# Kernel tuning notes

Hardware: AMD Instinct MI355X
Metric: run time of the kernel (lower is better)

## Reference

```python
import math
import jax, jax.numpy as jnp
import numpy as np

B, T, C = 4, 2048, 1024
N_HEAD = 16
HEAD_DIM = C // N_HEAD


def setup_inputs() -> dict:
    key = jax.random.key(0)
    k1, k2, k3 = jax.random.split(key, 3)
    x = jax.random.normal(k1, (B, T, C), dtype=jnp.float32)
    # nn.Linear weights: (out_features, in_features); init scale ~1/sqrt(C)
    w_attn = jax.random.normal(k2, (3 * C, C), dtype=jnp.float32) / math.sqrt(C)
    w_proj = jax.random.normal(k3, (C, C), dtype=jnp.float32) / math.sqrt(C)
    return {"x": x, "w_attn": w_attn, "w_proj": w_proj}


def reference(x, w_attn, w_proj):
    Bx, Tx, Cx = x.shape
    qkv = x @ w_attn.T  # (B,T,3C)
    q, k, v = jnp.split(qkv, 3, axis=2)
    # (B,T,H,D) -> (B,H,T,D)
    q = q.reshape(Bx, Tx, N_HEAD, HEAD_DIM).transpose(0, 2, 1, 3)
    k = k.reshape(Bx, Tx, N_HEAD, HEAD_DIM).transpose(0, 2, 1, 3)
    v = v.reshape(Bx, Tx, N_HEAD, HEAD_DIM).transpose(0, 2, 1, 3)
    scale = 1.0 / math.sqrt(HEAD_DIM)
    att = jnp.einsum("bhqd,bhkd->bhqk", q, k) * scale
    causal = jnp.tril(jnp.ones((Tx, Tx), dtype=bool))
    att = jnp.where(causal[None, None, :, :], att, -jnp.inf)
    att = jax.nn.softmax(att, axis=-1)
    out = jnp.einsum("bhqk,bhkd->bhqd", att, v)
    out = out.transpose(0, 2, 1, 3).reshape(Bx, Tx, Cx)
    return out @ w_proj.T
```

## Files before the change

kernel.cpp:

```cpp
#include <hip/hip_runtime.h>
#include <hip/hip_bf16.h>


typedef __attribute__((ext_vector_type(8))) short bf16x8;
typedef __attribute__((ext_vector_type(4))) float f32x4;
typedef unsigned short ushort_t;

#if __has_builtin(__builtin_amdgcn_exp2f)
#define EXP2(x) __builtin_amdgcn_exp2f(x)
#else
#define EXP2(x) exp2f(x)
#endif

__device__ inline ushort_t f2bf(float f) {
    union { float f; unsigned int u; } x; x.f = f;
    return (ushort_t)((x.u + 0x7fffu + ((x.u >> 16) & 1u)) >> 16);
}

__device__ inline ushort_t f2bf_fast(float f) {
    union { float f; unsigned int u; } x; x.f = f;
    return (ushort_t)((x.u + 0x8000u) >> 16);
}

__device__ inline bf16x8 load8_f32_to_bf16(const float* p) {
    float4 f0 = *(const float4*)p;
    float4 f1 = *(const float4*)(p + 4);
    bf16x8 r;
    r[0] = (short)f2bf(f0.x); r[1] = (short)f2bf(f0.y);
    r[2] = (short)f2bf(f0.z); r[3] = (short)f2bf(f0.w);
    r[4] = (short)f2bf(f1.x); r[5] = (short)f2bf(f1.y);
    r[6] = (short)f2bf(f1.z); r[7] = (short)f2bf(f1.w);
    return r;
}

__device__ inline void gl2lds16(const ushort_t* g, ushort_t* l) {
    __builtin_amdgcn_global_load_lds(
        (const __attribute__((address_space(1))) unsigned int*)g,
        (__attribute__((address_space(3))) unsigned int*)l,
        16, 0, 0);
}

__global__ void cvt3(const float* __restrict__ a, long n8a,
                     const float* __restrict__ b, long n8b,
                     const float* __restrict__ c, long n8c,
                     ushort_t* __restrict__ out) {
    long i = (long)blockIdx.x * 256 + threadIdx.x;
    const float* src; long off;
    if (i < n8a) { src = a; off = i; }
    else if (i < n8a + n8b) { src = b; off = i - n8a; }
    else if (i < n8a + n8b + n8c) { src = c; off = i - n8a - n8b; }
    else return;
    *(bf16x8*)(out + i * 8) = load8_f32_to_bf16(src + off * 8);
}

__global__ void fill_zero_f32(float* out, int n) {
    int i = blockIdx.x * 256 + threadIdx.x;
    if (i < n) out[i] = 0.0f;
}

#define QK_LOG2E_SCALE 0.18033688011112042f

#define PBK 32
#define PBUF 12288

template <int EPI>
__global__ __launch_bounds__(512) void gemm_np(
        const ushort_t* __restrict__ A, const ushort_t* __restrict__ B,
        void* __restrict__ Cp, void* __restrict__ Cp2,
        int M, int N, int K) {
    __shared__ ushort_t S[4 * PBUF];

    const int tid  = threadIdx.x;
    const int lane = tid & 63;
    const int w    = tid >> 6;
    const int quad = lane >> 4;
    const int l16  = lane & 15;
    const int wr   = w >> 2;
    const int wc   = w & 3;

    const int nbx = N >> 8;
    const int cpx = gridDim.x >> 3;
    const int swz = ((int)blockIdx.x & 7) * cpx + ((int)blockIdx.x >> 3);
    const int bm = (swz / nbx) << 7;
    const int bn = (swz % nbx) << 8;

    const int nt = K >> 5;

    const ushort_t* Ag = A + (size_t)(bm + w * 16 + (lane >> 2)) * K + (lane & 3) * 8;
    const ushort_t* Bg = B + (size_t)(bn + w * 16 + (lane >> 2)) * K + (lane & 3) * 8;
    const size_t rstep = (size_t)128 * K;

    auto stage = [&](int kt) {
        ushort_t* d = S + (kt & 3) * PBUF;
        const size_t ko = (size_t)kt * PBK;
        gl2lds16(Ag + ko,         d + w * 512);
        gl2lds16(Bg + ko,         d + 4096 + w * 512);
        gl2lds16(Bg + rstep + ko, d + 8192 + w * 512);
    };

    const int aoff = (wr * 64 + l16) * PBK + quad * 8;
    const int boff = 4096 + (wc * 64 + l16) * PBK + quad * 8;

    f32x4 acc[4][4] = {};

    stage(0); stage(1); stage(2);
    __asm__ __volatile__("s_waitcnt vmcnt(6)" ::: "memory");
    __builtin_amdgcn_s_barrier();

    for (int kt = 0; kt < nt; kt++) {
        if (kt + 3 < nt) stage(kt + 3);

        const ushort_t* Sb = S + (kt & 3) * PBUF;
        bf16x8 af[4], bfr[4];
#pragma unroll
        for (int i = 0; i < 4; i++)
            af[i]  = *(const bf16x8*)(Sb + aoff + i * (16 * PBK));
#pragma unroll
        for (int i = 0; i < 4; i++)
            bfr[i] = *(const bf16x8*)(Sb + boff + i * (16 * PBK));

        __builtin_amdgcn_s_setprio(1);
#pragma unroll
        for (int mi = 0; mi < 4; mi++)
#pragma unroll
            for (int ni = 0; ni < 4; ni++)
                acc[mi][ni] = __builtin_amdgcn_mfma_f32_16x16x32_bf16(
                    af[mi], bfr[ni], acc[mi][ni], 0, 0, 0);
        __builtin_amdgcn_s_setprio(0);

        if (kt + 3 < nt)
            __asm__ __volatile__("s_waitcnt vmcnt(6)" ::: "memory");
        else if (kt + 2 < nt)
            __asm__ __volatile__("s_waitcnt vmcnt(3)" ::: "memory");
        else if (kt + 1 < nt)
            __asm__ __volatile__("s_waitcnt vmcnt(0)" ::: "memory");
        __builtin_amdgcn_s_barrier();
    }

    const int colbase = bn + wc * 64;
    const int rowbase = bm + wr * 64 + quad * 4;
    if constexpr (EPI == 1) {
#pragma unroll
        for (int mi = 0; mi < 4; mi++) {
            const int row = rowbase + mi * 16;
            float* cr = (float*)Cp + (size_t)row * N + colbase + l16;
#pragma unroll
            for (int r = 0; r < 4; r++)
#pragma unroll
                for (int ni = 0; ni < 4; ni++)
                    cr[(size_t)r * N + ni * 16] = acc[mi][ni][r];
        }
    } else {
        if (colbase < 2048) {
            const float qs = (colbase < 1024) ? QK_LOG2E_SCALE : 1.0f;
#pragma unroll
            for (int mi = 0; mi < 4; mi++) {
                const int row = rowbase + mi * 16;
                ushort_t* qp = (ushort_t*)Cp + (size_t)row * 2048 + colbase + l16;
#pragma unroll
                for (int r = 0; r < 4; r++)
#pragma unroll
                    for (int ni = 0; ni < 4; ni++)
                        qp[(size_t)r * 2048 + ni * 16] = f2bf(acc[mi][ni][r] * qs);
            }
        } else {
#pragma unroll
            for (int mi = 0; mi < 4; mi++) {
                const int row = rowbase + mi * 16;
                const int bb = row >> 11, tt = row & 2047;
#pragma unroll
                for (int ni = 0; ni < 4; ni++) {
                    const int vc = colbase + ni * 16 + l16 - 2048;
                    const int hh = vc >> 6, dd = vc & 63;
                    ushort_t* vp = (ushort_t*)Cp2 +
                        ((((size_t)bb * 16 + hh) * 64 + dd) * 2048) + tt;
#pragma unroll
                    for (int r = 0; r < 4; r++)
                        vp[r] = f2bf(acc[mi][ni][r]);
                }
            }
        }
    }
}

#define BM 128
#define BN 128
#define BK 64
#define LDK 72

template <bool A_F32, bool B_F32, int EPI>
__global__ __launch_bounds__(256) void gemm_nt(
        const void* __restrict__ Ap, const void* __restrict__ Bp,
        void* __restrict__ Cp, void* __restrict__ Cp2,
        int M, int N, int K) {
    __shared__ ushort_t As[BM * LDK];
    __shared__ ushort_t Bs[BN * LDK];

    const int tid  = threadIdx.x;
    const int lane = tid & 63;
    const int w    = tid >> 6;
    const int quad = lane >> 4;
    const int l16  = lane & 15;

    const int bm = blockIdx.y * BM;
    const int bn = blockIdx.x * BN;
    const int wm = (w & 1) * 64;
    const int wn = (w >> 1) * 64;

    f32x4 acc[4][4] = {};

    const int lrow = tid >> 3;
    const int lcol = (tid & 7) * 8;

    bf16x8 pa[4], pb[4];
#pragma unroll
    for (int i = 0; i < 4; i++) {
        const int ra = lrow + i * 32;
        if constexpr (A_F32)
            pa[i] = load8_f32_to_bf16((const float*)Ap + (size_t)(bm + ra) * K + lcol);
        else
            pa[i] = *(const bf16x8*)((const ushort_t*)Ap + (size_t)(bm + ra) * K + lcol);
        if constexpr (B_F32)
            pb[i] = load8_f32_to_bf16((const float*)Bp + (size_t)(bn + ra) * K + lcol);
        else
            pb[i] = *(const bf16x8*)((const ushort_t*)Bp + (size_t)(bn + ra) * K + lcol);
    }

    for (int k0 = 0; k0 < K; k0 += BK) {
        __syncthreads();
#pragma unroll
        for (int i = 0; i < 4; i++) {
            *(bf16x8*)&As[(lrow + i * 32) * LDK + lcol] = pa[i];
            *(bf16x8*)&Bs[(lrow + i * 32) * LDK + lcol] = pb[i];
        }
        __syncthreads();

        if (k0 + BK < K) {
            const int kn = k0 + BK + lcol;
#pragma unroll
            for (int i = 0; i < 4; i++) {
                const int ra = lrow + i * 32;
                if constexpr (A_F32)
                    pa[i] = load8_f32_to_bf16((const float*)Ap + (size_t)(bm + ra) * K + kn);
                else
                    pa[i] = *(const bf16x8*)((const ushort_t*)Ap + (size_t)(bm + ra) * K + kn);
                if constexpr (B_F32)
                    pb[i] = load8_f32_to_bf16((const float*)Bp + (size_t)(bn + ra) * K + kn);
                else
                    pb[i] = *(const bf16x8*)((const ushort_t*)Bp + (size_t)(bn + ra) * K + kn);
            }
        }

#pragma unroll
        for (int ks = 0; ks < BK; ks += 32) {
            bf16x8 af[4], bfr[4];
#pragma unroll
            for (int i = 0; i < 4; i++)
                af[i] = *(const bf16x8*)&As[(wm + i * 16 + l16) * LDK + ks + quad * 8];
#pragma unroll
            for (int i = 0; i < 4; i++)
                bfr[i] = *(const bf16x8*)&Bs[(wn + i * 16 + l16) * LDK + ks + quad * 8];
#pragma unroll
            for (int mi = 0; mi < 4; mi++)
#pragma unroll
                for (int ni = 0; ni < 4; ni++)
                    acc[mi][ni] = __builtin_amdgcn_mfma_f32_16x16x32_bf16(
                        af[mi], bfr[ni], acc[mi][ni], 0, 0, 0);
        }
    }

#pragma unroll
    for (int mi = 0; mi < 4; mi++) {
        const int row0 = bm + wm + mi * 16 + quad * 4;
#pragma unroll
        for (int r = 0; r < 4; r++) {
            const int row = row0 + r;
            if constexpr (EPI == 1) {
                float* crow = (float*)Cp + (size_t)row * N + bn + wn;
#pragma unroll
                for (int ni = 0; ni < 4; ni++)
                    crow[ni * 16 + l16] = acc[mi][ni][r];
            } else {
                if (bn < 2048) {
                    const float qs = (bn < 1024) ? QK_LOG2E_SCALE : 1.0f;
                    ushort_t* crow = (ushort_t*)Cp + (size_t)row * 2048 + bn + wn;
#pragma unroll
                    for (int ni = 0; ni < 4; ni++)
                        crow[ni * 16 + l16] = f2bf(acc[mi][ni][r] * qs);
                } else {
                    ushort_t* vt = (ushort_t*)Cp2;
                    const int bb = row >> 11, tt = row & 2047;
#pragma unroll
                    for (int ni = 0; ni < 4; ni++) {
                        const int vc = bn + wn + ni * 16 + l16 - 2048;
                        const int hh = vc >> 6, dd = vc & 63;
                        vt[(((size_t)bb * 16 + hh) * 64 + dd) * 2048 + tt] =
                            f2bf(acc[mi][ni][r]);
                    }
                }
            }
        }
    }
}

#define AT_T 2048
#define PLD 72

__global__ __launch_bounds__(256) void attn4(
        const ushort_t* __restrict__ qk,
        const ushort_t* __restrict__ vt,
        ushort_t* __restrict__ attout) {
    const int bh   = blockIdx.x;
    const int qblk = (gridDim.y - 1) - blockIdx.y;
    const int b    = bh >> 4;
    const int h    = bh & 15;

    const int tid  = threadIdx.x;
    const int lane = tid & 63;
    const int w    = tid >> 6;
    const int quad = lane >> 4;
    const int l16  = lane & 15;
    const int sw   = l16 & 7;

    __shared__ ushort_t Ks[64 * 64];
    __shared__ ushort_t Vs[80 * 64];
    __shared__ ushort_t Ps[4][32 * PLD];

    for (int i = tid; i < 16 * 64; i += 256) Vs[64 * 64 + i] = 0;
    if (tid < 64) Vs[64 * 64 + tid] = 0x3F80;

    const ushort_t* qp = qk + (size_t)b * AT_T * 2048 + h * 64;
    const ushort_t* kp = qp + 1024;
    const ushort_t* vp = vt + (size_t)bh * 64 * 2048;

    const int Q0 = qblk * 128 + w * 16;

    bf16x8 aq[2][2];
#pragma unroll
    for (int s = 0; s < 2; s++) {
        const ushort_t* qrow = qp + (size_t)(Q0 + s * 64 + l16) * 2048;
        aq[s][0] = *(const bf16x8*)(qrow + quad * 8);
        aq[s][1] = *(const bf16x8*)(qrow + 32 + quad * 8);
    }

    f32x4 o[2][5] = {};

    const int lr8 = lane >> 3;
    const int cbg = ((lane & 7) ^ lr8) * 8;

    const int nk = 2 * qblk + 2;
    for (int kt = 0; kt < nk; kt++) {
        const int k0 = kt * 64;
        if (kt) __syncthreads();
#pragma unroll
        for (int j = 0; j < 2; j++) {
            gl2lds16(kp + (size_t)(k0 + w * 16 + j * 8 + lr8) * 2048 + cbg,
                     &Ks[(w * 16 + j * 8) * 64]);
            gl2lds16(vp + (size_t)(w * 16 + j * 8 + lr8) * 2048 + k0 + cbg,
                     &Vs[(w * 16 + j * 8) * 64]);
        }
        __syncthreads();

        f32x4 s0[4], s1[4];
#pragma unroll
        for (int c = 0; c < 4; c++) {
            s0[c][0] = -8.0f; s0[c][1] = -8.0f; s0[c][2] = -8.0f; s0[c][3] = -8.0f;
            s1[c] = s0[c];
#pragma unroll
            for (int ks = 0; ks < 2; ks++) {
                const int cs = ((quad + 4 * ks) ^ sw) * 8;
                bf16x8 bk = *(const bf16x8*)&Ks[(c * 16 + l16) * 64 + cs];
                s0[c] = __builtin_amdgcn_mfma_f32_16x16x32_bf16(aq[0][ks], bk, s0[c], 0, 0, 0);
                s1[c] = __builtin_amdgcn_mfma_f32_16x16x32_bf16(aq[1][ks], bk, s1[c], 0, 0, 0);
            }
        }

        if (kt >= 2 * qblk) {
            const int q0r = Q0 + quad * 4;
#pragma unroll
            for (int c = 0; c < 4; c++) {
                const int kcol = k0 + c * 16 + l16;
#pragma unroll
                for (int r = 0; r < 4; r++)
                    if (kcol > q0r + r) s0[c][r] = -__builtin_inff();
            }
        }
        if (kt == 2 * qblk + 1) {
            const int q1r = Q0 + 64 + quad * 4;
#pragma unroll
            for (int c = 0; c < 4; c++) {
                const int kcol = k0 + c * 16 + l16;
#pragma unroll
                for (int r = 0; r < 4; r++)
                    if (kcol > q1r + r) s1[c][r] = -__builtin_inff();
            }
        }

#pragma unroll
        for (int c = 0; c < 4; c++)
#pragma unroll
            for (int r = 0; r < 4; r++) {
                Ps[w][(quad * 4 + r) * PLD + c * 16 + l16] = f2bf_fast(EXP2(s0[c][r]));
                Ps[w][(16 + quad * 4 + r) * PLD + c * 16 + l16] = f2bf_fast(EXP2(s1[c][r]));
            }

        __asm__ __volatile__("s_waitcnt lgkmcnt(0)" ::: "memory");

#pragma unroll
        for (int ks = 0; ks < 2; ks++) {
            const int cs = ((quad + 4 * ks) ^ sw) * 8;
            bf16x8 ap0 = *(const bf16x8*)&Ps[w][l16 * PLD + ks * 32 + quad * 8];
            bf16x8 ap1 = *(const bf16x8*)&Ps[w][(16 + l16) * PLD + ks * 32 + quad * 8];
#pragma unroll
            for (int n = 0; n < 5; n++) {
                bf16x8 bv = *(const bf16x8*)&Vs[(n * 16 + l16) * 64 + cs];
                o[0][n] = __builtin_amdgcn_mfma_f32_16x16x32_bf16(ap0, bv, o[0][n], 0, 0, 0);
                o[1][n] = __builtin_amdgcn_mfma_f32_16x16x32_bf16(ap1, bv, o[1][n], 0, 0, 0);
            }
        }
    }

#pragma unroll
    for (int s = 0; s < 2; s++) {
        ushort_t* op = attout + (size_t)(b * AT_T + Q0 + s * 64 + quad * 4) * 1024 + h * 64;
#pragma unroll
        for (int r = 0; r < 4; r++) {
            const float l = __shfl(o[s][4][r], lane & 48, 64);
            const float inv = 1.0f / fmaxf(l, 1e-30f);
            ushort_t* orow = op + (size_t)r * 1024;
#pragma unroll
            for (int n = 0; n < 4; n++)
                orow[n * 16 + l16] = f2bf(o[s][n][r] * inv);
        }
    }
}

extern "C" void kernel_launch(void* const* d_in, const int* in_sizes, int n_in,
                              void* d_out, int out_size, void* d_ws, size_t ws_size,
                              hipStream_t stream) {
    const float* x      = (const float*)d_in[0];
    const float* w_attn = (const float*)d_in[1];
    const float* w_proj = (const float*)d_in[2];
    float* out = (float*)d_out;

    const int M = 8192, C = 1024;
    const size_t E_QK  = (size_t)M * 2048;
    const size_t E_VT  = (size_t)4 * 16 * 64 * 2048;
    const size_t E_ATT = (size_t)M * 1024;
    const size_t E_X   = (size_t)M * 1024;
    const size_t E_WA  = (size_t)3072 * 1024;
    const size_t E_WP  = (size_t)1024 * 1024;
    const size_t need_mid  = (E_QK + E_VT + E_ATT) * 2;
    const size_t need_full = need_mid + (E_X + E_WA + E_WP) * 2;

    if (ws_size < need_mid) {
        fill_zero_f32<<<(out_size + 255) / 256, 256, 0, stream>>>(out, out_size);
        return;
    }

    ushort_t* qk  = (ushort_t*)d_ws;
    ushort_t* vt  = qk + E_QK;
    ushort_t* att = vt + E_VT;

    if (ws_size >= need_full) {
        ushort_t* xb  = att + E_ATT;
        const long n8x = (long)(E_X / 8), n8a = (long)(E_WA / 8), n8p = (long)(E_WP / 8);
        const long n8  = n8x + n8a + n8p;
        cvt3<<<(int)((n8 + 255) / 256), 256, 0, stream>>>(
            x, n8x, w_attn, n8a, w_proj, n8p, xb);

        ushort_t* wab = xb + E_X;
        ushort_t* wpb = wab + E_WA;
        gemm_np<2><<<dim3((M / 128) * (3 * C / 256)), 512, 0, stream>>>(
            xb, wab, qk, vt, M, 3 * C, C);
        attn4<<<dim3(64, 16), 256, 0, stream>>>(qk, vt, att);
        gemm_np<1><<<dim3((M / 128) * (C / 256)), 512, 0, stream>>>(
            att, wpb, out, nullptr, M, C, C);
    } else {
        gemm_nt<true, true, 2><<<dim3(3 * C / BN, M / BM), 256, 0, stream>>>(
            x, w_attn, qk, vt, M, 3 * C, C);
        attn4<<<dim3(64, 16), 256, 0, stream>>>(qk, vt, att);
        gemm_nt<false, true, 1><<<dim3(C / BN, M / BM), 256, 0, stream>>>(
            att, w_proj, out, nullptr, M, C, C);
    }
}
```

Baseline: 238.7 us.

## Double GEMM K-tile to 64 with XOR-swizzled LDS and triple buffering

The bf16 GEMM now uses a K tile of 64 instead of 32 and keeps three LDS stages in flight instead of four. Each thread's global-to-LDS load target is XOR-swizzled by row, and reads use the matching swizzle to avoid LDS bank conflicts. This halves the barrier and wait count per K and doubles the MFMA work per iteration. In exchange it uses more LDS per block and prefetches one stage less deep.

After: 235.9 us. No clear change (-1.2%).

```diff
diff --git a/kernel.cpp b/kernel.cpp
--- a/kernel.cpp
+++ b/kernel.cpp
@@ -60,15 +60,17 @@
 
 #define QK_LOG2E_SCALE 0.18033688011112042f
 
-#define PBK 32
-#define PBUF 12288
+#define QBK 64
+#define ABUF (128 * 64)
+#define BBUF (256 * 64)
+#define TBUF (ABUF + BBUF)
 
 template <int EPI>
-__global__ __launch_bounds__(512) void gemm_np(
+__global__ __launch_bounds__(512) void gemm_sw(
         const ushort_t* __restrict__ A, const ushort_t* __restrict__ B,
         void* __restrict__ Cp, void* __restrict__ Cp2,
         int M, int N, int K) {
-    __shared__ ushort_t S[4 * PBUF];
+    __shared__ ushort_t S[3 * TBUF];
 
     const int tid  = threadIdx.x;
     const int lane = tid & 63;
@@ -84,57 +86,72 @@
     const int bm = (swz / nbx) << 7;
     const int bn = (swz % nbx) << 8;
 
-    const int nt = K >> 5;
-
-    const ushort_t* Ag = A + (size_t)(bm + w * 16 + (lane >> 2)) * K + (lane & 3) * 8;
-    const ushort_t* Bg = B + (size_t)(bn + w * 16 + (lane >> 2)) * K + (lane & 3) * 8;
-    const size_t rstep = (size_t)128 * K;
-
-    auto stage = [&](int kt) {
-        ushort_t* d = S + (kt & 3) * PBUF;
-        const size_t ko = (size_t)kt * PBK;
-        gl2lds16(Ag + ko,         d + w * 512);
-        gl2lds16(Bg + ko,         d + 4096 + w * 512);
-        gl2lds16(Bg + rstep + ko, d + 8192 + w * 512);
+    const int nt = K >> 6;
+
+    const int srow = lane >> 3;
+    const int soct = (lane & 7) ^ srow;
+    const ushort_t* Ag = A + (size_t)(bm + w * 16 + srow) * K + soct * 8;
+    const ushort_t* Bg = B + (size_t)(bn + w * 32 + srow) * K + soct * 8;
+
+    auto stage = [&](int kt, ushort_t* d) {
+        const size_t ko = (size_t)kt * QBK;
+        gl2lds16(Ag + ko,                  d + w * 1024);
+        gl2lds16(Ag + ko + (size_t)8 * K,  d + w * 1024 + 512);
+#pragma unroll
+        for (int j = 0; j < 4; j++)
+            gl2lds16(Bg + ko + (size_t)(j * 8) * K,
+                     d + ABUF + w * 2048 + j * 512);
     };
 
-    const int aoff = (wr * 64 + l16) * PBK + quad * 8;
-    const int boff = 4096 + (wc * 64 + l16) * PBK + quad * 8;
+    const int sl7 = l16 & 7;
+    const int ca0 = ((quad)     ^ sl7) * 8;
+    const int ca1 = ((quad + 4) ^ sl7) * 8;
+    const int arow = (wr * 64 + l16) * 64;
+    const int brow = ABUF + (wc * 64 + l16) * 64;
 
     f32x4 acc[4][4] = {};
 
-    stage(0); stage(1); stage(2);
+    stage(0, S);
+    stage(1, S + TBUF);
     __asm__ __volatile__("s_waitcnt vmcnt(6)" ::: "memory");
     __builtin_amdgcn_s_barrier();
 
+    int bc = 0, bs = 2;
     for (int kt = 0; kt < nt; kt++) {
-        if (kt + 3 < nt) stage(kt + 3);
-
-        const ushort_t* Sb = S + (kt & 3) * PBUF;
-        bf16x8 af[4], bfr[4];
-#pragma unroll
-        for (int i = 0; i < 4; i++)
-            af[i]  = *(const bf16x8*)(Sb + aoff + i * (16 * PBK));
-#pragma unroll
-        for (int i = 0; i < 4; i++)
-            bfr[i] = *(const bf16x8*)(Sb + boff + i * (16 * PBK));
+        if (kt + 2 < nt) stage(kt + 2, S + bs * TBUF);
+
+        const ushort_t* Sb = S + bc * TBUF;
+        bf16x8 af[4][2], bfr[4][2];
+#pragma unroll
+        for (int mi = 0; mi < 4; mi++) {
+            af[mi][0] = *(const bf16x8*)(Sb + arow + mi * 1024 + ca0);
+            af[mi][1] = *(const bf16x8*)(Sb + arow + mi * 1024 + ca1);
+        }
+#pragma unroll
+        for (int ni = 0; ni < 4; ni++) {
+            bfr[ni][0] = *(const bf16x8*)(Sb + brow + ni * 1024 + ca0);
+            bfr[ni][1] = *(const bf16x8*)(Sb + brow + ni * 1024 + ca1);
+        }
 
         __builtin_amdgcn_s_setprio(1);
 #pragma unroll
         for (int mi = 0; mi < 4; mi++)
 #pragma unroll
             for (int ni = 0; ni < 4; ni++)
-                acc[mi][ni] = __builtin_amdgcn_mfma_f32_16x16x32_bf16(
-                    af[mi], bfr[ni], acc[mi][ni], 0, 0, 0);
+#pragma unroll
+                for (int kk = 0; kk < 2; kk++)
+                    acc[mi][ni] = __builtin_amdgcn_mfma_f32_16x16x32_bf16(
+                        af[mi][kk], bfr[ni][kk], acc[mi][ni], 0, 0, 0);
         __builtin_amdgcn_s_setprio(0);
 
-        if (kt + 3 < nt)
+        if (kt + 2 < nt)
             __asm__ __volatile__("s_waitcnt vmcnt(6)" ::: "memory");
-        else if (kt + 2 < nt)
-            __asm__ __volatile__("s_waitcnt vmcnt(3)" ::: "memory");
         else if (kt + 1 < nt)
             __asm__ __volatile__("s_waitcnt vmcnt(0)" ::: "memory");
         __builtin_amdgcn_s_barrier();
+
+        bc = (bc + 1 == 3) ? 0 : bc + 1;
+        bs = (bs + 1 == 3) ? 0 : bs + 1;
     }
 
     const int colbase = bn + wc * 64;
@@ -471,10 +488,10 @@
 
         ushort_t* wab = xb + E_X;
         ushort_t* wpb = wab + E_WA;
-        gemm_np<2><<<dim3((M / 128) * (3 * C / 256)), 512, 0, stream>>>(
+        gemm_sw<2><<<dim3((M / 128) * (3 * C / 256)), 512, 0, stream>>>(
             xb, wab, qk, vt, M, 3 * C, C);
         attn4<<<dim3(64, 16), 256, 0, stream>>>(qk, vt, att);
-        gemm_np<1><<<dim3((M / 128) * (C / 256)), 512, 0, stream>>>(
+        gemm_sw<1><<<dim3((M / 128) * (C / 256)), 512, 0, stream>>>(
             att, wpb, out, nullptr, M, C, C);
     } else {
         gemm_nt<true, true, 2><<<dim3(3 * C / BN, M / BM), 256, 0, stream>>>(
```
